# Kernel optimization log

Measured on AMD Instinct MI355X. Metric: run time of the kernel, lower is better.

The kernel has to match this reference:

```python
import jax, jax.numpy as jnp
import numpy as np

N_NODES = 100000
N_EDGES = 1600000
IN_DIM = 128
OUT_DIM = 32
N_HEADS = 4


def setup_inputs() -> dict:
    key = jax.random.key(0)
    k1, k2, k3, k4, k5 = jax.random.split(key, 5)
    x = jax.random.normal(k1, (N_NODES, IN_DIM), dtype=jnp.float32)
    edge_index = jax.random.randint(k2, (2, N_EDGES), 0, N_NODES, dtype=jnp.int64)
    # torch nn.Linear weight layout: [out_features, in_features]
    W = jax.random.normal(k3, (OUT_DIM * N_HEADS, IN_DIM), dtype=jnp.float32) * (1.0 / np.sqrt(IN_DIM))
    a_left = jax.random.normal(k4, (N_HEADS, OUT_DIM), dtype=jnp.float32) * 0.01
    a_right = jax.random.normal(k5, (N_HEADS, OUT_DIM), dtype=jnp.float32) * 0.01
    return {"x": x, "edge_index": edge_index, "W": W, "a_left": a_left, "a_right": a_right}


def reference(x, edge_index, W, a_left, a_right):
    N = x.shape[0]
    H, D = a_left.shape
    # h: [N, H, D]
    h = (x @ W.T).reshape(N, H, D)
    src = edge_index[0]
    dst = edge_index[1]
    h_src = h[src]                                   # [E, H, D] gather
    h_dst = h[dst]                                   # [E, H, D] gather
    e = jnp.einsum('ehd,hd->eh', h_src, a_left) + jnp.einsum('ehd,hd->eh', h_dst, a_right)
    e = jax.nn.leaky_relu(e, negative_slope=0.2)
    e_exp = jnp.exp(e)                               # faithful: no max-subtraction, as in source
    denom = jax.ops.segment_sum(e_exp, dst, num_segments=N)   # [N, H]
    alpha = e_exp / (denom[dst] + 1e-8)              # [E, H]
    weighted = h_src * alpha[:, :, None]             # [E, H, D]
    out = jax.ops.segment_sum(weighted, dst, num_segments=N)  # [N, H, D]
    return out.reshape(N, H * D)                     # concat=True
```

## Files before the change

kernel.cpp:

```cpp
#include <hip/hip_runtime.h>
#include <hip/hip_bf16.h>


constexpr int IN_DIM = 128;
constexpr int HD     = 128;
constexpr int CSHIFT = 10;
constexpr int CCAP   = 17408;
constexpr int CPAD   = 16;

__device__ __forceinline__ unsigned short f2bf(float f) {
  __hip_bfloat16 b = __float2bfloat16(f);
  return *(unsigned short*)&b;
}
__device__ __forceinline__ float bfl(unsigned u) { return __uint_as_float(u << 16); }
__device__ __forceinline__ float bfh(unsigned u) { return __uint_as_float(u & 0xffff0000u); }

__global__ __launch_bounds__(256)
void gemm_k(const float* __restrict__ x, const float* __restrict__ W,
            const float* __restrict__ a_left, const float* __restrict__ a_right,
            unsigned int* __restrict__ hb,
            float* __restrict__ el, float* __restrict__ er,
            int N) {
  __shared__ float xs[32][132];
  __shared__ float ws[32][132];
  const int tid = threadIdx.x;
  const int tx = tid & 15, ty = tid >> 4;
  const int n0 = blockIdx.x * 128;

  float acc[8][8];
#pragma unroll
  for (int i = 0; i < 8; ++i)
#pragma unroll
    for (int j = 0; j < 8; ++j) acc[i][j] = 0.f;

  for (int kc = 0; kc < IN_DIM; kc += 32) {
#pragma unroll
    for (int i = 0; i < 4; ++i) {
      int f  = tid + 256 * i;
      int r  = f >> 3;
      int k4 = f & 7;
      float4 xv = make_float4(0.f, 0.f, 0.f, 0.f);
      int node = n0 + r;
      if (node < N) xv = *(const float4*)&x[(size_t)node * IN_DIM + kc + 4 * k4];
      xs[4*k4+0][r] = xv.x; xs[4*k4+1][r] = xv.y; xs[4*k4+2][r] = xv.z; xs[4*k4+3][r] = xv.w;
      float4 wv = *(const float4*)&W[(size_t)r * IN_DIM + kc + 4 * k4];
      ws[4*k4+0][r] = wv.x; ws[4*k4+1][r] = wv.y; ws[4*k4+2][r] = wv.z; ws[4*k4+3][r] = wv.w;
    }
    __syncthreads();
#pragma unroll 8
    for (int kk = 0; kk < 32; ++kk) {
      float4 xa = *(const float4*)&xs[kk][8 * ty];
      float4 xb = *(const float4*)&xs[kk][8 * ty + 4];
      float4 wa = *(const float4*)&ws[kk][4 * tx];
      float4 wb = *(const float4*)&ws[kk][64 + 4 * tx];
      float xr[8] = {xa.x, xa.y, xa.z, xa.w, xb.x, xb.y, xb.z, xb.w};
      float wr[8] = {wa.x, wa.y, wa.z, wa.w, wb.x, wb.y, wb.z, wb.w};
#pragma unroll
      for (int i = 0; i < 8; ++i)
#pragma unroll
        for (int j = 0; j < 8; ++j) acc[i][j] += xr[i] * wr[j];
    }
    __syncthreads();
  }

  const int headA = tx >> 3;
  const int headB = 2 + (tx >> 3);
  const int co    = 4 * (tx & 7);
  float alA[4], arA[4], alB[4], arB[4];
#pragma unroll
  for (int j = 0; j < 4; ++j) {
    alA[j] = a_left [headA * 32 + co + j];
    arA[j] = a_right[headA * 32 + co + j];
    alB[j] = a_left [headB * 32 + co + j];
    arB[j] = a_right[headB * 32 + co + j];
  }
#pragma unroll
  for (int i = 0; i < 8; ++i) {
    int node = n0 + 8 * ty + i;
    if (node < N) {
      uint2 pA, pB;
      pA.x = ((unsigned)f2bf(acc[i][1]) << 16) | f2bf(acc[i][0]);
      pA.y = ((unsigned)f2bf(acc[i][3]) << 16) | f2bf(acc[i][2]);
      pB.x = ((unsigned)f2bf(acc[i][5]) << 16) | f2bf(acc[i][4]);
      pB.y = ((unsigned)f2bf(acc[i][7]) << 16) | f2bf(acc[i][6]);
      *(uint2*)&hb[(size_t)node * 64 + 2 * tx]      = pA;
      *(uint2*)&hb[(size_t)node * 64 + 32 + 2 * tx] = pB;
      float plA = 0.f, prA = 0.f, plB = 0.f, prB = 0.f;
#pragma unroll
      for (int j = 0; j < 4; ++j) {
        plA += acc[i][j]     * alA[j];  prA += acc[i][j]     * arA[j];
        plB += acc[i][4 + j] * alB[j];  prB += acc[i][4 + j] * arB[j];
      }
#pragma unroll
      for (int m = 1; m < 8; m <<= 1) {
        plA += __shfl_xor(plA, m, 64);  prA += __shfl_xor(prA, m, 64);
        plB += __shfl_xor(plB, m, 64);  prB += __shfl_xor(prB, m, 64);
      }
      if ((tx & 7) == 0) {
        el[node * 4 + headA] = plA;  er[node * 4 + headA] = prA;
        el[node * 4 + headB] = plB;  er[node * 4 + headB] = prB;
      }
    }
  }
}

__global__ __launch_bounds__(1024)
void binA_k(const int* __restrict__ ei, int* __restrict__ ccnt,
            unsigned* __restrict__ c1buf, int E, int ncb) {
  __shared__ unsigned staged[8192];
  __shared__ unsigned short sbin[8192];
  __shared__ int hist[128], loff[128], cur[128], gbase[128];
  __shared__ int lws[2];
  const int t = threadIdx.x;
  const int base = blockIdx.x * 8192;

  if (t < 128) hist[t] = 0;
  __syncthreads();

  int src[8], dst[8], bin[8];
#pragma unroll
  for (int i = 0; i < 8; ++i) {
    int e = base + t + 1024 * i;
    if (e < E) {
      src[i] = ei[e];
      dst[i] = ei[E + e];
      bin[i] = dst[i] >> CSHIFT;
      atomicAdd(&hist[bin[i]], 1);
    } else bin[i] = -1;
  }
  __syncthreads();

  int v = 0, s = 0;
  if (t < 128) {
    v = hist[t]; s = v;
#pragma unroll
    for (int d = 1; d < 64; d <<= 1) {
      int u = __shfl_up(s, d, 64);
      if ((t & 63) >= d) s += u;
    }
    if ((t & 63) == 63) lws[t >> 6] = s;
  }
  __syncthreads();
  if (t < 128) {
    int prefix = (t >= 64) ? lws[0] : 0;
    int excl = prefix + s - v;
    loff[t] = excl;
    cur[t]  = excl;
    gbase[t] = (t < ncb && v > 0) ? atomicAdd(&ccnt[t * CPAD], v) : 0;
  }
  __syncthreads();

#pragma unroll
  for (int i = 0; i < 8; ++i) {
    if (bin[i] >= 0) {
      int p = atomicAdd(&cur[bin[i]], 1);
      staged[p] = (unsigned)src[i] | ((unsigned)(dst[i] & 1023) << 17);
      sbin[p]   = (unsigned short)bin[i];
    }
  }
  __syncthreads();

  const int tot = loff[127] + hist[127];
  for (int j = t; j < tot; j += 1024) {
    int b = sbin[j];
    int pos = gbase[b] + (j - loff[b]);
    if (pos < CCAP) c1buf[(size_t)b * CCAP + pos] = staged[j];
  }
}

__global__ __launch_bounds__(128)
void cscan_k(const int* __restrict__ ccnt, int* __restrict__ cbase,
             int* __restrict__ offsets, int ncb, int N, int E) {
  __shared__ int lws[2];
  const int t = threadIdx.x;
  int v = (t < ncb) ? ccnt[t * CPAD] : 0;
  int s = v;
#pragma unroll
  for (int d = 1; d < 64; d <<= 1) {
    int u = __shfl_up(s, d, 64);
    if ((t & 63) >= d) s += u;
  }
  if ((t & 63) == 63) lws[t >> 6] = s;
  __syncthreads();
  int prefix = (t >= 64) ? lws[0] : 0;
  if (t < ncb) cbase[t] = prefix + s - v;
  if (t == 0) offsets[N] = E;
}

__global__ __launch_bounds__(1024)
void binB_k(const unsigned* __restrict__ c1buf, const int* __restrict__ ccnt,
            const int* __restrict__ cbase, int* __restrict__ offsets,
            int* __restrict__ csr, int N) {
  __shared__ int hist[1024];
  __shared__ int wsum[16];
  const int b = blockIdx.x, t = threadIdx.x;
  int m = ccnt[b * CPAD];
  if (m > CCAP) m = CCAP;
  const int gb = cbase[b];
  hist[t] = 0;
  __syncthreads();
  const unsigned* bp = c1buf + (size_t)b * CCAP;
  for (int i = t; i < m; i += 1024) atomicAdd(&hist[bp[i] >> 17], 1);
  __syncthreads();
  int v = hist[t], s = v;
#pragma unroll
  for (int d = 1; d < 64; d <<= 1) {
    int u = __shfl_up(s, d, 64);
    if ((t & 63) >= d) s += u;
  }
  if ((t & 63) == 63) wsum[t >> 6] = s;
  __syncthreads();
  int prefix = 0;
  for (int w = 0; w < (t >> 6); ++w) prefix += wsum[w];
  int excl = prefix + s - v;
  int node = (b << CSHIFT) + t;
  if (node < N) offsets[node] = gb + excl;
  hist[t] = excl;
  __syncthreads();
  for (int i = t; i < m; i += 1024) {
    unsigned u = bp[i];
    int r = atomicAdd(&hist[u >> 17], 1);
    csr[gb + r] = (int)(u & 0x1FFFFu);
  }
}

__global__ __launch_bounds__(256)
void agg_k(const uint4* __restrict__ hb4, const float* __restrict__ el,
           const float* __restrict__ er, const int* __restrict__ offsets,
           const int* __restrict__ csr, float* __restrict__ out, int N) {
  const int wid  = (blockIdx.x * blockDim.x + threadIdx.x) >> 6;
  const int lane = threadIdx.x & 63;
  if (wid >= N) return;
  const int start = offsets[wid];
  const int end   = offsets[wid + 1];
  const int q    = lane >> 4;
  const int ql   = lane & 15;
  const int head = ql >> 2;
  const float erv = er[wid * 4 + head];

  float a0=0.f,a1=0.f,a2=0.f,a3=0.f,a4=0.f,a5=0.f,a6=0.f,a7=0.f,den=0.f;
  for (int k = start; k < end; k += 4) {
    int e  = k + q;
    int ec = (e < end) ? e : (end - 1);
    int sN = csr[ec];
    float elv = el[sN * 4 + head];
    float t = elv + erv;
    t = (t > 0.f) ? t : 0.2f * t;
    float w = __expf(t);
    if (e >= end) w = 0.f;
    uint4 hv = hb4[(size_t)sN * 16 + ql];
    a0 += w * bfl(hv.x);  a1 += w * bfh(hv.x);
    a2 += w * bfl(hv.y);  a3 += w * bfh(hv.y);
    a4 += w * bfl(hv.z);  a5 += w * bfh(hv.z);
    a6 += w * bfl(hv.w);  a7 += w * bfh(hv.w);
    den += w;
  }
#pragma unroll
  for (int m = 16; m < 64; m <<= 1) {
    a0 += __shfl_xor(a0, m, 64);  a1 += __shfl_xor(a1, m, 64);
    a2 += __shfl_xor(a2, m, 64);  a3 += __shfl_xor(a3, m, 64);
    a4 += __shfl_xor(a4, m, 64);  a5 += __shfl_xor(a5, m, 64);
    a6 += __shfl_xor(a6, m, 64);  a7 += __shfl_xor(a7, m, 64);
    den += __shfl_xor(den, m, 64);
  }
  if (q == 0) {
    float inv = 1.f / (den + 1e-8f);
    float4 o0 = make_float4(a0 * inv, a1 * inv, a2 * inv, a3 * inv);
    float4 o1 = make_float4(a4 * inv, a5 * inv, a6 * inv, a7 * inv);
    *(float4*)&out[(size_t)wid * HD + 8 * ql]     = o0;
    *(float4*)&out[(size_t)wid * HD + 8 * ql + 4] = o1;
  }
}

extern "C" void kernel_launch(void* const* d_in, const int* in_sizes, int n_in,
                              void* d_out, int out_size, void* d_ws, size_t ws_size,
                              hipStream_t stream) {
  const float* x       = (const float*)d_in[0];
  const int*   ei      = (const int*)d_in[1];
  const float* W       = (const float*)d_in[2];
  const float* a_left  = (const float*)d_in[3];
  const float* a_right = (const float*)d_in[4];
  float* out = (float*)d_out;

  const int N = in_sizes[0] / IN_DIM;
  const int E = in_sizes[1] / 2;
  const int NCB = (N + 1023) >> CSHIFT;

  char* p = (char*)d_ws;
  unsigned int* hb = (unsigned int*)p; p += (size_t)N * 64 * sizeof(unsigned int);
  float* el      = (float*)p; p += (size_t)N * 4 * sizeof(float);
  float* er      = (float*)p; p += (size_t)N * 4 * sizeof(float);
  int*   offsets = (int*)p;   p += (size_t)(N + 1) * sizeof(int);
  int*   ccnt    = (int*)p;   p += (size_t)NCB * CPAD * sizeof(int);
  int*   cbase   = (int*)p;   p += (size_t)NCB * sizeof(int);
  int*   csr     = (int*)p;   p += (size_t)E * sizeof(int);
  unsigned* c1buf = (unsigned*)p; p += (size_t)NCB * CCAP * sizeof(unsigned);

  hipMemsetAsync(ccnt, 0, (size_t)NCB * CPAD * sizeof(int), stream);

  gemm_k<<<(N + 127) / 128, 256, 0, stream>>>(x, W, a_left, a_right, hb, el, er, N);
  binA_k<<<(E + 8191) / 8192, 1024, 0, stream>>>(ei, ccnt, c1buf, E, NCB);
  cscan_k<<<1, 128, 0, stream>>>(ccnt, cbase, offsets, NCB, N, E);
  binB_k<<<NCB, 1024, 0, stream>>>(c1buf, ccnt, cbase, offsets, csr, N);
  agg_k<<<(N + 3) / 4, 256, 0, stream>>>((const uint4*)hb, el, er, offsets, csr, out, N);
}
```

Measured before the change: 268.1 us.

## Fuse bucket scan into binB and batch CSR loads with 2-edge unroll in aggregation

Removes the single-block cscan kernel by having every binB block recompute the 98-entry bucket prefix scan redundantly, saving one launch and a serialization point. The aggregation loop now loads 64 CSR indices per wave in one coalesced nontemporal load and broadcasts them with shuffles. It processes two edges per quarter-wave per iteration to raise memory-level parallelism for the gathers. Output stores become nontemporal. The cost is more registers and a tail path with masking.

```diff
diff --git a/kernel.cpp b/kernel.cpp
--- a/kernel.cpp
+++ b/kernel.cpp
@@ -7,6 +7,8 @@
 constexpr int CSHIFT = 10;
 constexpr int CCAP   = 17408;
 constexpr int CPAD   = 16;
+
+typedef float f32x4 __attribute__((ext_vector_type(4)));
 
 __device__ __forceinline__ unsigned short f2bf(float f) {
   __hip_bfloat16 b = __float2bfloat16(f);
@@ -168,37 +170,39 @@
   }
 }
 
-__global__ __launch_bounds__(128)
-void cscan_k(const int* __restrict__ ccnt, int* __restrict__ cbase,
-             int* __restrict__ offsets, int ncb, int N, int E) {
-  __shared__ int lws[2];
-  const int t = threadIdx.x;
-  int v = (t < ncb) ? ccnt[t * CPAD] : 0;
-  int s = v;
-#pragma unroll
-  for (int d = 1; d < 64; d <<= 1) {
-    int u = __shfl_up(s, d, 64);
-    if ((t & 63) >= d) s += u;
-  }
-  if ((t & 63) == 63) lws[t >> 6] = s;
-  __syncthreads();
-  int prefix = (t >= 64) ? lws[0] : 0;
-  if (t < ncb) cbase[t] = prefix + s - v;
-  if (t == 0) offsets[N] = E;
-}
-
 __global__ __launch_bounds__(1024)
 void binB_k(const unsigned* __restrict__ c1buf, const int* __restrict__ ccnt,
-            const int* __restrict__ cbase, int* __restrict__ offsets,
-            int* __restrict__ csr, int N) {
+            int* __restrict__ offsets, int* __restrict__ csr,
+            int N, int ncb, int E) {
   __shared__ int hist[1024];
   __shared__ int wsum[16];
+  __shared__ int lws2[2];
+  __shared__ int sgb;
   const int b = blockIdx.x, t = threadIdx.x;
   int m = ccnt[b * CPAD];
   if (m > CCAP) m = CCAP;
-  const int gb = cbase[b];
   hist[t] = 0;
-  __syncthreads();
+
+  int cv = 0, cs = 0;
+  if (t < 128) {
+    cv = (t < ncb) ? ccnt[t * CPAD] : 0;
+    cs = cv;
+#pragma unroll
+    for (int d = 1; d < 64; d <<= 1) {
+      int u = __shfl_up(cs, d, 64);
+      if ((t & 63) >= d) cs += u;
+    }
+    if ((t & 63) == 63) lws2[t >> 6] = cs;
+  }
+  if (t == 0 && b == 0) offsets[N] = E;
+  __syncthreads();
+  if (t < 128) {
+    int prefix = (t >= 64) ? lws2[0] : 0;
+    if (t == b) sgb = prefix + cs - cv;
+  }
+  __syncthreads();
+  const int gb = sgb;
+
   const unsigned* bp = c1buf + (size_t)b * CCAP;
   for (int i = t; i < m; i += 1024) atomicAdd(&hist[bp[i] >> 17], 1);
   __syncthreads();
@@ -239,22 +243,58 @@
   const float erv = er[wid * 4 + head];
 
   float a0=0.f,a1=0.f,a2=0.f,a3=0.f,a4=0.f,a5=0.f,a6=0.f,a7=0.f,den=0.f;
-  for (int k = start; k < end; k += 4) {
-    int e  = k + q;
-    int ec = (e < end) ? e : (end - 1);
-    int sN = csr[ec];
-    float elv = el[sN * 4 + head];
-    float t = elv + erv;
-    t = (t > 0.f) ? t : 0.2f * t;
-    float w = __expf(t);
-    if (e >= end) w = 0.f;
-    uint4 hv = hb4[(size_t)sN * 16 + ql];
-    a0 += w * bfl(hv.x);  a1 += w * bfh(hv.x);
-    a2 += w * bfl(hv.y);  a3 += w * bfh(hv.y);
-    a4 += w * bfl(hv.z);  a5 += w * bfh(hv.z);
-    a6 += w * bfl(hv.w);  a7 += w * bfh(hv.w);
-    den += w;
-  }
+
+  for (int base = start; base < end; base += 64) {
+    int lim = end - base; if (lim > 64) lim = 64;
+    int ce  = base + lane;
+    int creg = __builtin_nontemporal_load(&csr[(ce < end) ? ce : (end - 1)]);
+
+    int i = 0;
+    for (; i + 8 <= lim; i += 8) {
+      int s0 = __shfl(creg, i + q, 64);
+      int s1 = __shfl(creg, i + 4 + q, 64);
+      uint4 h0 = hb4[(size_t)s0 * 16 + ql];
+      uint4 h1 = hb4[(size_t)s1 * 16 + ql];
+      float e0 = el[s0 * 4 + head];
+      float e1 = el[s1 * 4 + head];
+      float t0 = e0 + erv; t0 = (t0 > 0.f) ? t0 : 0.2f * t0;
+      float t1 = e1 + erv; t1 = (t1 > 0.f) ? t1 : 0.2f * t1;
+      float w0 = __expf(t0), w1 = __expf(t1);
+      a0 += w0 * bfl(h0.x) + w1 * bfl(h1.x);
+      a1 += w0 * bfh(h0.x) + w1 * bfh(h1.x);
+      a2 += w0 * bfl(h0.y) + w1 * bfl(h1.y);
+      a3 += w0 * bfh(h0.y) + w1 * bfh(h1.y);
+      a4 += w0 * bfl(h0.z) + w1 * bfl(h1.z);
+      a5 += w0 * bfh(h0.z) + w1 * bfh(h1.z);
+      a6 += w0 * bfl(h0.w) + w1 * bfl(h1.w);
+      a7 += w0 * bfh(h0.w) + w1 * bfh(h1.w);
+      den += w0 + w1;
+    }
+    if (i < lim) {
+      int i0 = i + q, i1 = i + 4 + q;
+      int s0 = __shfl(creg, (i0 < lim) ? i0 : 0, 64);
+      int s1 = __shfl(creg, (i1 < lim) ? i1 : 0, 64);
+      uint4 h0 = hb4[(size_t)s0 * 16 + ql];
+      uint4 h1 = hb4[(size_t)s1 * 16 + ql];
+      float e0 = el[s0 * 4 + head];
+      float e1 = el[s1 * 4 + head];
+      float t0 = e0 + erv; t0 = (t0 > 0.f) ? t0 : 0.2f * t0;
+      float t1 = e1 + erv; t1 = (t1 > 0.f) ? t1 : 0.2f * t1;
+      float w0 = __expf(t0), w1 = __expf(t1);
+      if (i0 >= lim) w0 = 0.f;
+      if (i1 >= lim) w1 = 0.f;
+      a0 += w0 * bfl(h0.x) + w1 * bfl(h1.x);
+      a1 += w0 * bfh(h0.x) + w1 * bfh(h1.x);
+      a2 += w0 * bfl(h0.y) + w1 * bfl(h1.y);
+      a3 += w0 * bfh(h0.y) + w1 * bfh(h1.y);
+      a4 += w0 * bfl(h0.z) + w1 * bfl(h1.z);
+      a5 += w0 * bfh(h0.z) + w1 * bfh(h1.z);
+      a6 += w0 * bfl(h0.w) + w1 * bfl(h1.w);
+      a7 += w0 * bfh(h0.w) + w1 * bfh(h1.w);
+      den += w0 + w1;
+    }
+  }
+
 #pragma unroll
   for (int m = 16; m < 64; m <<= 1) {
     a0 += __shfl_xor(a0, m, 64);  a1 += __shfl_xor(a1, m, 64);
@@ -265,10 +305,10 @@
   }
   if (q == 0) {
     float inv = 1.f / (den + 1e-8f);
-    float4 o0 = make_float4(a0 * inv, a1 * inv, a2 * inv, a3 * inv);
-    float4 o1 = make_float4(a4 * inv, a5 * inv, a6 * inv, a7 * inv);
-    *(float4*)&out[(size_t)wid * HD + 8 * ql]     = o0;
-    *(float4*)&out[(size_t)wid * HD + 8 * ql + 4] = o1;
+    f32x4 o0 = {a0 * inv, a1 * inv, a2 * inv, a3 * inv};
+    f32x4 o1 = {a4 * inv, a5 * inv, a6 * inv, a7 * inv};
+    __builtin_nontemporal_store(o0, (f32x4*)&out[(size_t)wid * HD + 8 * ql]);
+    __builtin_nontemporal_store(o1, (f32x4*)&out[(size_t)wid * HD + 8 * ql + 4]);
   }
 }
 
@@ -292,7 +332,6 @@
   float* er      = (float*)p; p += (size_t)N * 4 * sizeof(float);
   int*   offsets = (int*)p;   p += (size_t)(N + 1) * sizeof(int);
   int*   ccnt    = (int*)p;   p += (size_t)NCB * CPAD * sizeof(int);
-  int*   cbase   = (int*)p;   p += (size_t)NCB * sizeof(int);
   int*   csr     = (int*)p;   p += (size_t)E * sizeof(int);
   unsigned* c1buf = (unsigned*)p; p += (size_t)NCB * CCAP * sizeof(unsigned);
 
@@ -300,7 +339,6 @@
 
   gemm_k<<<(N + 127) / 128, 256, 0, stream>>>(x, W, a_left, a_right, hb, el, er, N);
   binA_k<<<(E + 8191) / 8192, 1024, 0, stream>>>(ei, ccnt, c1buf, E, NCB);
-  cscan_k<<<1, 128, 0, stream>>>(ccnt, cbase, offsets, NCB, N, E);
-  binB_k<<<NCB, 1024, 0, stream>>>(c1buf, ccnt, cbase, offsets, csr, N);
+  binB_k<<<NCB, 1024, 0, stream>>>(c1buf, ccnt, offsets, csr, N, NCB, E);
   agg_k<<<(N + 3) / 4, 256, 0, stream>>>((const uint4*)hb, el, er, offsets, csr, out, N);
 }
```

After: 259.3 us. -3.3%, faster.
